# Optimization experiments

Measured on AMD Instinct MI355X. Metric: run time of the kernel, lower is better.

## Reference

```python
import jax, jax.numpy as jnp
import numpy as np

N = 100000      # nodes
E = 3200000     # edges (avg degree 32)
F_IN = 500      # input features
HID = 8         # per-head hidden dim (layer 1)
HEADS = 8       # heads (layer 1)
NC = 41         # num classes (layer 2, 1 head)


def setup_inputs() -> dict:
    key = jax.random.key(0)
    ks = jax.random.split(key, 8)
    x = jax.random.normal(ks[0], (N, F_IN), jnp.float32)
    edge_index = jax.random.randint(ks[1], (2, E), 0, N, dtype=jnp.int64)
    W1 = jax.random.normal(ks[2], (F_IN, HEADS * HID), jnp.float32) / np.sqrt(F_IN)
    a1_src = jax.random.normal(ks[3], (HEADS, HID), jnp.float32) / np.sqrt(HID)
    a1_dst = jax.random.normal(ks[4], (HEADS, HID), jnp.float32) / np.sqrt(HID)
    W2 = jax.random.normal(ks[5], (HEADS * HID, NC), jnp.float32) / np.sqrt(HEADS * HID)
    a2_src = jax.random.normal(ks[6], (1, NC), jnp.float32) / np.sqrt(NC)
    a2_dst = jax.random.normal(ks[7], (1, NC), jnp.float32) / np.sqrt(NC)
    return {"x": x, "edge_index": edge_index, "W1": W1, "a1_src": a1_src,
            "a1_dst": a1_dst, "W2": W2, "a2_src": a2_src, "a2_dst": a2_dst}


def gat_layer(x, edge_index, W, a_src, a_dst, heads, out_dim, concat):
    n = x.shape[0]
    h = (x @ W).reshape(n, heads, out_dim)                    # [N,H,D]
    # per-node attention halves (avoids gathering full features for logits)
    alpha_src = jnp.einsum('nhd,hd->nh', h, a_src)            # [N,H]
    alpha_dst = jnp.einsum('nhd,hd->nh', h, a_dst)            # [N,H]
    src, dst = edge_index[0], edge_index[1]
    e = jax.nn.leaky_relu(alpha_src[src] + alpha_dst[dst], 0.2)  # [E,H]
    # segment softmax over incoming edges of each destination node
    e_max = jax.lax.stop_gradient(jax.ops.segment_max(e, dst, num_segments=n))
    e_exp = jnp.exp(e - e_max[dst])
    denom = jax.ops.segment_sum(e_exp, dst, num_segments=n)
    alpha = e_exp / (denom[dst] + 1e-16)                      # [E,H]
    msg = alpha[:, :, None] * h[src]                          # [E,H,D]
    out = jax.ops.segment_sum(msg, dst, num_segments=n)       # [N,H,D]
    return out.reshape(n, heads * out_dim) if concat else out.mean(axis=1)


def reference(x, edge_index, W1, a1_src, a1_dst, W2, a2_src, a2_dst):
    # dropout layers are identity at inference
    h = gat_layer(x, edge_index, W1, a1_src, a1_dst, HEADS, HID, True)   # [N,64]
    h = jax.nn.elu(h)
    out = gat_layer(h, edge_index, W2, a2_src, a2_dst, 1, NC, False)     # [N,41]
    return jax.nn.log_softmax(out, axis=1)
```

## Files before the change

### kernel.cpp

```cpp
#include <hip/hip_runtime.h>
#include <hip/hip_bf16.h>
#include <math.h>


#define DEV __device__ __forceinline__

constexpr int N_NODES = 100000;
constexpr int N_EDGES = 3200000;
constexpr int F_IN    = 500;
constexpr int HEADS   = 8;
constexpr int HID     = 8;
constexpr int D1      = HEADS * HID;
constexpr int NC      = 41;

constexpr int NB    = 196;
constexpr int BCAP  = 20480;
constexpr int SEPT  = 16;
constexpr int SCHUNK = 256 * SEPT;

constexpr int KPAD  = 512;
constexpr int LROW  = 520;

constexpr int WSTR = 68;

typedef __attribute__((ext_vector_type(8))) short bf16x8;
typedef __attribute__((ext_vector_type(4))) float f32x4;

DEV float bf2f(unsigned short u) {
    return __uint_as_float(((unsigned int)u) << 16);
}
DEV unsigned short f2b(float f) {
    unsigned int u = __float_as_uint(f);
    unsigned int r = (u + 0x7FFFu + ((u >> 16) & 1u)) >> 16;
    return (unsigned short)r;
}
DEV float leaky(float e) { return e > 0.f ? e : 0.2f * e; }
DEV float readlane_f(float v, int l) {
    return __uint_as_float((unsigned int)__builtin_amdgcn_readlane((int)__float_as_uint(v), l));
}

__global__ void k_detect_convert(const void* xraw, const void* eraw,
                                 const void* w1, const void* a1s, const void* a1d,
                                 const void* w2, const void* a2s, const void* a2d,
                                 unsigned short* W1frag, float* A1Sf, float* A1Df,
                                 float* W2f, float* A2Sf, float* A2Df,
                                 int* flags) {
    __shared__ int sf;
    if (threadIdx.x == 0) {
        const unsigned short* xu = (const unsigned short*)xraw;
        int valid = 0;
        for (int i = 0; i < 64; i++) {
            unsigned short v = xu[2 * i];
            int e = (v >> 7) & 0xFF;
            if (e == 0 || (e >= 90 && e <= 150)) valid++;
        }
        int xf32 = (valid < 56) ? 1 : 0;
        const unsigned int* eu = (const unsigned int*)eraw;
        int zeros = 0;
        for (int k = 0; k < 64; k++)
            if (eu[2 * k + 1] == 0u) zeros++;
        int e64 = (zeros == 64) ? 1 : 0;
        flags[0] = xf32;
        flags[1] = e64;
        sf = xf32;
    }
    __syncthreads();
    bool f32 = (sf != 0);
    auto conv = [&](const void* src, float* dst, int n) {
        if (f32) {
            const float* s = (const float*)src;
            for (int i = threadIdx.x; i < n; i += blockDim.x) dst[i] = s[i];
        } else {
            const unsigned short* s = (const unsigned short*)src;
            for (int i = threadIdx.x; i < n; i += blockDim.x) dst[i] = bf2f(s[i]);
        }
    };
    conv(a1s, A1Sf, HEADS * HID);
    conv(a1d, A1Df, HEADS * HID);
    conv(w2, W2f, D1 * NC);
    conv(a2s, A2Sf, NC);
    conv(a2d, A2Df, NC);
    for (int idx = threadIdx.x; idx < 4 * 16 * 64 * 8; idx += blockDim.x) {
        int wid = idx >> 13, kb = (idx >> 9) & 15, ln = (idx >> 3) & 63, j = idx & 7;
        int k = kb * 32 + (ln >> 4) * 8 + j;
        int n = wid * 16 + (ln & 15);
        unsigned short bits = 0;
        if (k < F_IN) {
            if (f32) bits = f2b(((const float*)w1)[k * D1 + n]);
            else     bits = ((const unsigned short*)w1)[k * D1 + n];
        }
        W1frag[idx] = bits;
    }
}

__global__ __launch_bounds__(256) void k_bucket_scatter(const void* eraw, const int* flags,
                                                        int* bucket_cnt, unsigned int* staging) {
    __shared__ int bh[NB];
    const int t = threadIdx.x;
    for (int i = t; i < NB; i += 256) bh[i] = 0;
    __syncthreads();
    const bool e64 = flags[1] != 0;
    const unsigned int* eu = (const unsigned int*)eraw;
    const int e0 = blockIdx.x * SCHUNK;
    int sv[SEPT], dv[SEPT];
#pragma unroll
    for (int k = 0; k < SEPT; k++) {
        int i = e0 + k * 256 + t;
        if (i < N_EDGES) {
            if (e64) { sv[k] = (int)eu[2 * i]; dv[k] = (int)eu[2 * (N_EDGES + i)]; }
            else     { sv[k] = (int)eu[i];     dv[k] = (int)eu[N_EDGES + i]; }
            atomicAdd(&bh[dv[k] >> 9], 1);
        } else dv[k] = -1;
    }
    __syncthreads();
    for (int i = t; i < NB; i += 256) {
        int c = bh[i];
        int base = c ? atomicAdd(&bucket_cnt[i], c) : 0;
        bh[i] = i * BCAP + base;
    }
    __syncthreads();
#pragma unroll
    for (int k = 0; k < SEPT; k++) {
        if (dv[k] >= 0) {
            int b = dv[k] >> 9;
            int slot = atomicAdd(&bh[b], 1);
            staging[slot] = (unsigned)sv[k] | ((unsigned)(dv[k] & 511) << 17);
        }
    }
}

__global__ void k_cscan(const int* bucket_cnt, int* cbase, int* off) {
    __shared__ int s[256];
    int t = threadIdx.x;
    s[t] = (t < NB) ? bucket_cnt[t] : 0;
    __syncthreads();
    for (int o = 1; o < 256; o <<= 1) {
        int v = (t >= o) ? s[t - o] : 0;
        __syncthreads();
        s[t] += v;
        __syncthreads();
    }
    if (t < NB) cbase[t + 1] = s[t];
    if (t == 0) { cbase[0] = 0; off[N_NODES] = N_EDGES; }
}

__global__ __launch_bounds__(512) void k_csr_build(const unsigned int* __restrict__ staging,
                                                   const int* __restrict__ bucket_cnt,
                                                   const int* __restrict__ cbase,
                                                   int* __restrict__ off, int* __restrict__ csr) {
    __shared__ int sdeg[512];
    __shared__ int scur[512];
    const int t = threadIdx.x;
    const int b = blockIdx.x;
    const int n0 = b << 9;
    const int start = b * BCAP;
    const int end = start + bucket_cnt[b];
    const int base = cbase[b];
    sdeg[t] = 0;
    __syncthreads();
    for (int i = start + t; i < end; i += 512)
        atomicAdd(&sdeg[staging[i] >> 17], 1);
    __syncthreads();
    int d = sdeg[t];
    for (int o = 1; o < 512; o <<= 1) {
        int v = (t >= o) ? sdeg[t - o] : 0;
        __syncthreads();
        sdeg[t] += v;
        __syncthreads();
    }
    int excl = sdeg[t] - d;
    if (n0 + t < N_NODES) off[n0 + t] = base + excl;
    scur[t] = base + excl;
    __syncthreads();
    for (int i = start + t; i < end; i += 512) {
        unsigned v = staging[i];
        int slot = atomicAdd(&scur[v >> 17], 1);
        csr[slot] = (int)(v & 0x1FFFFu);
    }
}

__global__ __launch_bounds__(256) void k_gemm1(const void* xraw, const int* flags,
                                               const unsigned short* __restrict__ W1frag,
                                               const float* A1Sf, const float* A1Df,
                                               unsigned short* __restrict__ h1b,
                                               float* __restrict__ as1,
                                               float* __restrict__ ad1) {
    __shared__ unsigned short ldsx[64 * LROW];
    const int t = threadIdx.x;
    const int r0 = blockIdx.x * 64;
    const bool xf32 = flags[0] != 0;
#pragma unroll
    for (int it = 0; it < 32; it++) {
        int s = it * 256 + t;
        int row = s >> 7, c4 = s & 127;
        int row_g = r0 + row;
        ushort4 v = make_ushort4(0, 0, 0, 0);
        if (c4 < 125 && row_g < N_NODES) {
            if (xf32) {
                float4 f = *(const float4*)((const float*)xraw + (size_t)row_g * F_IN + c4 * 4);
                v = make_ushort4(f2b(f.x), f2b(f.y), f2b(f.z), f2b(f.w));
            } else {
                v = *(const ushort4*)((const unsigned short*)xraw + (size_t)row_g * F_IN + c4 * 4);
            }
        }
        *(ushort4*)(ldsx + row * LROW + c4 * 4) = v;
    }
    __syncthreads();

    const int lane = t & 63;
    const int wid = __builtin_amdgcn_readfirstlane(t >> 6);
    const int m = lane & 15, q = lane >> 4;
    f32x4 acc[4] = {{0.f, 0.f, 0.f, 0.f}, {0.f, 0.f, 0.f, 0.f},
                    {0.f, 0.f, 0.f, 0.f}, {0.f, 0.f, 0.f, 0.f}};
    const unsigned short* wf = W1frag + (size_t)wid * 8192;
#pragma unroll 4
    for (int kb = 0; kb < 16; kb++) {
        bf16x8 b = *(const bf16x8*)(wf + (kb * 64 + lane) * 8);
#pragma unroll
        for (int mb = 0; mb < 4; mb++) {
            bf16x8 a = *(const bf16x8*)(ldsx + (mb * 16 + m) * LROW + kb * 32 + q * 8);
            acc[mb] = __builtin_amdgcn_mfma_f32_16x16x32_bf16(a, b, acc[mb], 0, 0, 0);
        }
    }
    const int col = wid * 16 + m;
    const float a_s = A1Sf[col], a_d = A1Df[col];
    const int h = 2 * wid + (m >> 3);
#pragma unroll
    for (int mb = 0; mb < 4; mb++) {
#pragma unroll
        for (int reg = 0; reg < 4; reg++) {
            int gr = r0 + mb * 16 + q * 4 + reg;
            float vacc = acc[mb][reg];
            bool ok = gr < N_NODES;
            if (ok) h1b[(size_t)gr * D1 + col] = f2b(vacc);
            float ts = vacc * a_s, td = vacc * a_d;
            ts += __shfl_xor(ts, 1, 64); td += __shfl_xor(td, 1, 64);
            ts += __shfl_xor(ts, 2, 64); td += __shfl_xor(td, 2, 64);
            ts += __shfl_xor(ts, 4, 64); td += __shfl_xor(td, 4, 64);
            if (ok && (lane & 7) == 0) {
                as1[gr * HEADS + h] = ts;
                ad1[gr * HEADS + h] = td;
            }
        }
    }
}

__global__ __launch_bounds__(256) void k_agg1(const int* __restrict__ csr,
                                              const int* __restrict__ off,
                                              const unsigned short* __restrict__ h1b,
                                              const float* __restrict__ as1,
                                              const float* __restrict__ ad1,
                                              float* __restrict__ h1e) {
    __shared__ float wlds[4][8 * WSTR];
    const int t = threadIdx.x;
    const int lane = t & 63;
    const int n = (blockIdx.x * blockDim.x + t) >> 6;
    if (n >= N_NODES) return;
    const int beg = off[n], end = off[n + 1];
    const int h0 = lane >> 3;
    float* wl = wlds[(t >> 6) & 3];
    const float* wrow = wl + h0 * WSTR;
    const float* adp = ad1 + n * HEADS;
    float acc = 0.f, dsum = 0.f;
    for (int base = beg; base < end; base += 64) {
        const int cnt = min(64, end - base);
        int sl = 0;
        if (lane < cnt) {
            sl = csr[base + lane];
            const float* ap = as1 + sl * HEADS;
            float4 aa = *(const float4*)(ap);
            float4 ab = *(const float4*)(ap + 4);
            wl[0 * WSTR + lane] = __expf(leaky(aa.x + adp[0]));
            wl[1 * WSTR + lane] = __expf(leaky(aa.y + adp[1]));
            wl[2 * WSTR + lane] = __expf(leaky(aa.z + adp[2]));
            wl[3 * WSTR + lane] = __expf(leaky(aa.w + adp[3]));
            wl[4 * WSTR + lane] = __expf(leaky(ab.x + adp[4]));
            wl[5 * WSTR + lane] = __expf(leaky(ab.y + adp[5]));
            wl[6 * WSTR + lane] = __expf(leaky(ab.z + adp[6]));
            wl[7 * WSTR + lane] = __expf(leaky(ab.w + adp[7]));
        }
        asm volatile("s_waitcnt lgkmcnt(0)" ::: "memory");
        int j = 0;
        for (; j + 4 <= cnt; j += 4) {
            int s0 = __builtin_amdgcn_readlane(sl, j);
            int s1 = __builtin_amdgcn_readlane(sl, j + 1);
            int s2 = __builtin_amdgcn_readlane(sl, j + 2);
            int s3 = __builtin_amdgcn_readlane(sl, j + 3);
            float4 wv = *(const float4*)(wrow + j);
            float g0 = bf2f(h1b[(size_t)s0 * D1 + lane]);
            float g1 = bf2f(h1b[(size_t)s1 * D1 + lane]);
            float g2 = bf2f(h1b[(size_t)s2 * D1 + lane]);
            float g3 = bf2f(h1b[(size_t)s3 * D1 + lane]);
            acc = fmaf(wv.x, g0, acc); dsum += wv.x;
            acc = fmaf(wv.y, g1, acc); dsum += wv.y;
            acc = fmaf(wv.z, g2, acc); dsum += wv.z;
            acc = fmaf(wv.w, g3, acc); dsum += wv.w;
        }
        for (; j < cnt; j++) {
            int s = __builtin_amdgcn_readlane(sl, j);
            float w = wrow[j];
            acc = fmaf(w, bf2f(h1b[(size_t)s * D1 + lane]), acc);
            dsum += w;
        }
    }
    float v = acc / (dsum + 1e-16f);
    float o = v > 0.f ? v : (__expf(v) - 1.f);
    h1e[(size_t)n * D1 + lane] = o;
}

__global__ __launch_bounds__(256) void k_gemm2(const float* __restrict__ h1e,
                                               const float* __restrict__ W2f,
                                               const float* __restrict__ A2Sf,
                                               const float* __restrict__ A2Df,
                                               unsigned short* __restrict__ h2b,
                                               float* __restrict__ as2,
                                               float* __restrict__ ad2) {
    const int row = blockIdx.x * blockDim.x + threadIdx.x;
    if (row >= N_NODES) return;
    float acc[NC];
#pragma unroll
    for (int c = 0; c < NC; c++) acc[c] = 0.f;
    const float* xr = h1e + (size_t)row * D1;
    for (int k = 0; k < D1; k += 4) {
        float4 hv = *(const float4*)(xr + k);
#pragma unroll
        for (int c = 0; c < NC; c++) {
            acc[c] = fmaf(hv.x, W2f[(k + 0) * NC + c], acc[c]);
            acc[c] = fmaf(hv.y, W2f[(k + 1) * NC + c], acc[c]);
            acc[c] = fmaf(hv.z, W2f[(k + 2) * NC + c], acc[c]);
            acc[c] = fmaf(hv.w, W2f[(k + 3) * NC + c], acc[c]);
        }
    }
    float ts = 0.f, td = 0.f;
#pragma unroll
    for (int c = 0; c < NC; c++) {
        h2b[(size_t)row * NC + c] = f2b(acc[c]);
        ts = fmaf(acc[c], A2Sf[c], ts);
        td = fmaf(acc[c], A2Df[c], td);
    }
    as2[row] = ts;
    ad2[row] = td;
}

__global__ __launch_bounds__(256) void k_agg2(const int* __restrict__ csr,
                                              const int* __restrict__ off,
                                              const unsigned short* __restrict__ h2b,
                                              const float* __restrict__ as2,
                                              const float* __restrict__ ad2,
                                              const int* flags, void* out) {
    const int lane = threadIdx.x & 63;
    const int n = (blockIdx.x * blockDim.x + threadIdx.x) >> 6;
    if (n >= N_NODES) return;
    const int beg = off[n], end = off[n + 1];
    const float ad = ad2[n];
    const bool act = lane < NC;
    const int cl = act ? lane : 0;
    float acc = 0.f, dsum = 0.f;
    for (int base = beg; base < end; base += 64) {
        const int cnt = min(64, end - base);
        int idx = min(base + lane, N_EDGES - 1);
        int sl = csr[idx];
        float w = __expf(leaky(as2[sl] + ad));
        int j = 0;
        for (; j + 4 <= cnt; j += 4) {
            int s0 = __builtin_amdgcn_readlane(sl, j);
            int s1 = __builtin_amdgcn_readlane(sl, j + 1);
            int s2 = __builtin_amdgcn_readlane(sl, j + 2);
            int s3 = __builtin_amdgcn_readlane(sl, j + 3);
            float w0 = readlane_f(w, j);
            float w1 = readlane_f(w, j + 1);
            float w2 = readlane_f(w, j + 2);
            float w3 = readlane_f(w, j + 3);
            float g0 = bf2f(h2b[(size_t)s0 * NC + cl]);
            float g1 = bf2f(h2b[(size_t)s1 * NC + cl]);
            float g2 = bf2f(h2b[(size_t)s2 * NC + cl]);
            float g3 = bf2f(h2b[(size_t)s3 * NC + cl]);
            acc = fmaf(w0, g0, acc); dsum += w0;
            acc = fmaf(w1, g1, acc); dsum += w1;
            acc = fmaf(w2, g2, acc); dsum += w2;
            acc = fmaf(w3, g3, acc); dsum += w3;
        }
        for (; j < cnt; j++) {
            int s = __builtin_amdgcn_readlane(sl, j);
            float wj = readlane_f(w, j);
            acc = fmaf(wj, bf2f(h2b[(size_t)s * NC + cl]), acc);
            dsum += wj;
        }
    }
    float val = acc / (dsum + 1e-16f);
    float v = act ? val : -INFINITY;
    float m = v;
#pragma unroll
    for (int o = 1; o < 64; o <<= 1) m = fmaxf(m, __shfl_xor(m, o, 64));
    float ex = act ? __expf(val - m) : 0.f;
#pragma unroll
    for (int o = 1; o < 64; o <<= 1) ex += __shfl_xor(ex, o, 64);
    float res = val - m - __logf(ex);
    if (act) {
        if (flags[0])
            ((float*)out)[(size_t)n * NC + lane] = res;
        else
            ((__hip_bfloat16*)out)[(size_t)n * NC + lane] = __float2bfloat16(res);
    }
}

extern "C" void kernel_launch(void* const* d_in, const int* in_sizes, int n_in,
                              void* d_out, int out_size, void* d_ws, size_t ws_size,
                              hipStream_t stream) {
    char* p = (char*)d_ws;
    auto alloc = [&](size_t bytes) -> void* {
        void* r = (void*)p;
        p += (bytes + 255) & ~(size_t)255;
        return r;
    };
    int* flags  = (int*)alloc(16);
    unsigned short* W1frag = (unsigned short*)alloc(4 * 16 * 64 * 8 * 2);
    float* A1Sf = (float*)alloc(HEADS * HID * 4);
    float* A1Df = (float*)alloc(HEADS * HID * 4);
    float* W2f  = (float*)alloc((size_t)D1 * NC * 4);
    float* A2Sf = (float*)alloc(NC * 4);
    float* A2Df = (float*)alloc(NC * 4);
    unsigned short* h1b = (unsigned short*)alloc((size_t)N_NODES * D1 * 2);
    float* as1  = (float*)alloc((size_t)N_NODES * HEADS * 4);
    float* ad1  = (float*)alloc((size_t)N_NODES * HEADS * 4);
    float* h1e  = (float*)alloc((size_t)N_NODES * D1 * 4);
    unsigned short* h2b = (unsigned short*)alloc((size_t)N_NODES * NC * 2);
    float* as2  = (float*)alloc((size_t)N_NODES * 4);
    float* ad2  = (float*)alloc((size_t)N_NODES * 4);
    int* off    = (int*)alloc((size_t)(N_NODES + 1) * 4);
    int* csr    = (int*)alloc((size_t)N_EDGES * 4);
    int* bucket_cnt = (int*)alloc((size_t)NB * 4);
    int* cbase      = (int*)alloc((size_t)(NB + 1) * 4);
    unsigned int* staging = (unsigned int*)h1e;

    hipMemsetAsync(bucket_cnt, 0, (size_t)NB * 4, stream);

    k_detect_convert<<<1, 256, 0, stream>>>(d_in[0], d_in[1], d_in[2], d_in[3],
                                            d_in[4], d_in[5], d_in[6], d_in[7],
                                            W1frag, A1Sf, A1Df, W2f, A2Sf, A2Df, flags);
    k_bucket_scatter<<<(N_EDGES + SCHUNK - 1) / SCHUNK, 256, 0, stream>>>(d_in[1], flags, bucket_cnt, staging);
    k_cscan<<<1, 256, 0, stream>>>(bucket_cnt, cbase, off);
    k_csr_build<<<NB, 512, 0, stream>>>(staging, bucket_cnt, cbase, off, csr);

    k_gemm1<<<1563, 256, 0, stream>>>(d_in[0], flags, W1frag, A1Sf, A1Df, h1b, as1, ad1);
    k_agg1<<<25000, 256, 0, stream>>>(csr, off, h1b, as1, ad1, h1e);
    k_gemm2<<<391, 256, 0, stream>>>(h1e, W2f, A2Sf, A2Df, h2b, as2, ad2);
    k_agg2<<<25000, 256, 0, stream>>>(csr, off, h2b, as2, ad2, flags, d_out);
}
```

Measured before the change: 696.8 us.

## Split detect/convert into parallel kernels and retile gemm1 to 32-row blocks

```diff
diff --git a/kernel.cpp b/kernel.cpp
--- a/kernel.cpp
+++ b/kernel.cpp
@@ -18,7 +18,7 @@
 constexpr int SEPT  = 16;
 constexpr int SCHUNK = 256 * SEPT;
 
-constexpr int KPAD  = 512;
+constexpr int GROWS = 32;
 constexpr int LROW  = 520;
 
 constexpr int WSTR = 68;
@@ -39,48 +39,44 @@
     return __uint_as_float((unsigned int)__builtin_amdgcn_readlane((int)__float_as_uint(v), l));
 }
 
-__global__ void k_detect_convert(const void* xraw, const void* eraw,
-                                 const void* w1, const void* a1s, const void* a1d,
-                                 const void* w2, const void* a2s, const void* a2d,
-                                 unsigned short* W1frag, float* A1Sf, float* A1Df,
-                                 float* W2f, float* A2Sf, float* A2Df,
-                                 int* flags) {
-    __shared__ int sf;
-    if (threadIdx.x == 0) {
-        const unsigned short* xu = (const unsigned short*)xraw;
-        int valid = 0;
-        for (int i = 0; i < 64; i++) {
-            unsigned short v = xu[2 * i];
-            int e = (v >> 7) & 0xFF;
-            if (e == 0 || (e >= 90 && e <= 150)) valid++;
-        }
-        int xf32 = (valid < 56) ? 1 : 0;
-        const unsigned int* eu = (const unsigned int*)eraw;
-        int zeros = 0;
-        for (int k = 0; k < 64; k++)
-            if (eu[2 * k + 1] == 0u) zeros++;
-        int e64 = (zeros == 64) ? 1 : 0;
-        flags[0] = xf32;
-        flags[1] = e64;
-        sf = xf32;
-    }
-    __syncthreads();
-    bool f32 = (sf != 0);
-    auto conv = [&](const void* src, float* dst, int n) {
-        if (f32) {
-            const float* s = (const float*)src;
-            for (int i = threadIdx.x; i < n; i += blockDim.x) dst[i] = s[i];
-        } else {
-            const unsigned short* s = (const unsigned short*)src;
-            for (int i = threadIdx.x; i < n; i += blockDim.x) dst[i] = bf2f(s[i]);
-        }
-    };
-    conv(a1s, A1Sf, HEADS * HID);
-    conv(a1d, A1Df, HEADS * HID);
-    conv(w2, W2f, D1 * NC);
-    conv(a2s, A2Sf, NC);
-    conv(a2d, A2Df, NC);
-    for (int idx = threadIdx.x; idx < 4 * 16 * 64 * 8; idx += blockDim.x) {
+__global__ void k_detect(const void* xraw, const void* eraw, int* flags) {
+    const int lane = threadIdx.x & 63;
+    const unsigned short* xu = (const unsigned short*)xraw;
+    unsigned short v = xu[2 * lane];
+    int e = (v >> 7) & 0xFF;
+    int valid = (e == 0 || (e >= 90 && e <= 150)) ? 1 : 0;
+    unsigned long long vm = __ballot(valid);
+    const unsigned int* eu = (const unsigned int*)eraw;
+    unsigned long long zm = __ballot(eu[2 * lane + 1] == 0u);
+    if (lane == 0) {
+        flags[0] = (__popcll(vm) < 56) ? 1 : 0;
+        flags[1] = (__popcll(zm) == 64) ? 1 : 0;
+    }
+}
+
+__global__ __launch_bounds__(256) void k_convert(const void* w1, const void* a1s, const void* a1d,
+                                                 const void* w2, const void* a2s, const void* a2d,
+                                                 const int* flags,
+                                                 unsigned short* W1frag, float* A1Sf, float* A1Df,
+                                                 float* W2f, float* A2Sf, float* A2Df) {
+    const bool f32 = flags[0] != 0;
+    if (blockIdx.x == 0) {
+        auto conv = [&](const void* src, float* dst, int n) {
+            if (f32) {
+                const float* s = (const float*)src;
+                for (int i = threadIdx.x; i < n; i += blockDim.x) dst[i] = s[i];
+            } else {
+                const unsigned short* s = (const unsigned short*)src;
+                for (int i = threadIdx.x; i < n; i += blockDim.x) dst[i] = bf2f(s[i]);
+            }
+        };
+        conv(a1s, A1Sf, HEADS * HID);
+        conv(a1d, A1Df, HEADS * HID);
+        conv(w2, W2f, D1 * NC);
+        conv(a2s, A2Sf, NC);
+        conv(a2d, A2Df, NC);
+    }
+    for (int idx = blockIdx.x * 256 + threadIdx.x; idx < 4 * 16 * 64 * 8; idx += 64 * 256) {
         int wid = idx >> 13, kb = (idx >> 9) & 15, ln = (idx >> 3) & 63, j = idx & 7;
         int k = kb * 32 + (ln >> 4) * 8 + j;
         int n = wid * 16 + (ln & 15);
@@ -179,23 +175,23 @@
     }
 }
 
-__global__ __launch_bounds__(256) void k_gemm1(const void* xraw, const int* flags,
-                                               const unsigned short* __restrict__ W1frag,
-                                               const float* A1Sf, const float* A1Df,
-                                               unsigned short* __restrict__ h1b,
-                                               float* __restrict__ as1,
-                                               float* __restrict__ ad1) {
-    __shared__ unsigned short ldsx[64 * LROW];
+__global__ __launch_bounds__(512, 8) void k_gemm1(const void* xraw, const int* flags,
+                                                  const unsigned short* __restrict__ W1frag,
+                                                  const float* A1Sf, const float* A1Df,
+                                                  unsigned short* __restrict__ h1b,
+                                                  float* __restrict__ as1,
+                                                  float* __restrict__ ad1) {
+    __shared__ unsigned short ldsx[GROWS * LROW];
     const int t = threadIdx.x;
-    const int r0 = blockIdx.x * 64;
+    const int r0 = blockIdx.x * GROWS;
     const bool xf32 = flags[0] != 0;
-#pragma unroll
-    for (int it = 0; it < 32; it++) {
-        int s = it * 256 + t;
+#pragma unroll 4
+    for (int it = 0; it < 8; it++) {
+        int s = it * 512 + t;
         int row = s >> 7, c4 = s & 127;
         int row_g = r0 + row;
         ushort4 v = make_ushort4(0, 0, 0, 0);
-        if (c4 < 125 && row_g < N_NODES) {
+        if (c4 < 125) {
             if (xf32) {
                 float4 f = *(const float4*)((const float*)xraw + (size_t)row_g * F_IN + c4 * 4);
                 v = make_ushort4(f2b(f.x), f2b(f.y), f2b(f.z), f2b(f.w));
@@ -208,39 +204,34 @@
     __syncthreads();
 
     const int lane = t & 63;
-    const int wid = __builtin_amdgcn_readfirstlane(t >> 6);
+    const int w = t >> 6;
+    const int wid = __builtin_amdgcn_readfirstlane(w & 3);
+    const int mb  = __builtin_amdgcn_readfirstlane(w >> 2);
     const int m = lane & 15, q = lane >> 4;
-    f32x4 acc[4] = {{0.f, 0.f, 0.f, 0.f}, {0.f, 0.f, 0.f, 0.f},
-                    {0.f, 0.f, 0.f, 0.f}, {0.f, 0.f, 0.f, 0.f}};
+    f32x4 acc = {0.f, 0.f, 0.f, 0.f};
     const unsigned short* wf = W1frag + (size_t)wid * 8192;
+    const unsigned short* arow = ldsx + (mb * 16 + m) * LROW + q * 8;
 #pragma unroll 4
     for (int kb = 0; kb < 16; kb++) {
         bf16x8 b = *(const bf16x8*)(wf + (kb * 64 + lane) * 8);
-#pragma unroll
-        for (int mb = 0; mb < 4; mb++) {
-            bf16x8 a = *(const bf16x8*)(ldsx + (mb * 16 + m) * LROW + kb * 32 + q * 8);
-            acc[mb] = __builtin_amdgcn_mfma_f32_16x16x32_bf16(a, b, acc[mb], 0, 0, 0);
-        }
+        bf16x8 a = *(const bf16x8*)(arow + kb * 32);
+        acc = __builtin_amdgcn_mfma_f32_16x16x32_bf16(a, b, acc, 0, 0, 0);
     }
     const int col = wid * 16 + m;
     const float a_s = A1Sf[col], a_d = A1Df[col];
     const int h = 2 * wid + (m >> 3);
 #pragma unroll
-    for (int mb = 0; mb < 4; mb++) {
-#pragma unroll
-        for (int reg = 0; reg < 4; reg++) {
-            int gr = r0 + mb * 16 + q * 4 + reg;
-            float vacc = acc[mb][reg];
-            bool ok = gr < N_NODES;
-            if (ok) h1b[(size_t)gr * D1 + col] = f2b(vacc);
-            float ts = vacc * a_s, td = vacc * a_d;
-            ts += __shfl_xor(ts, 1, 64); td += __shfl_xor(td, 1, 64);
-            ts += __shfl_xor(ts, 2, 64); td += __shfl_xor(td, 2, 64);
-            ts += __shfl_xor(ts, 4, 64); td += __shfl_xor(td, 4, 64);
-            if (ok && (lane & 7) == 0) {
-                as1[gr * HEADS + h] = ts;
-                ad1[gr * HEADS + h] = td;
-            }
+    for (int reg = 0; reg < 4; reg++) {
+        int gr = r0 + mb * 16 + q * 4 + reg;
+        float vacc = acc[reg];
+        h1b[(size_t)gr * D1 + col] = f2b(vacc);
+        float ts = vacc * a_s, td = vacc * a_d;
+        ts += __shfl_xor(ts, 1, 64); td += __shfl_xor(td, 1, 64);
+        ts += __shfl_xor(ts, 2, 64); td += __shfl_xor(td, 2, 64);
+        ts += __shfl_xor(ts, 4, 64); td += __shfl_xor(td, 4, 64);
+        if ((lane & 7) == 0) {
+            as1[gr * HEADS + h] = ts;
+            ad1[gr * HEADS + h] = td;
         }
     }
 }
@@ -435,14 +426,14 @@
 
     hipMemsetAsync(bucket_cnt, 0, (size_t)NB * 4, stream);
 
-    k_detect_convert<<<1, 256, 0, stream>>>(d_in[0], d_in[1], d_in[2], d_in[3],
-                                            d_in[4], d_in[5], d_in[6], d_in[7],
-                                            W1frag, A1Sf, A1Df, W2f, A2Sf, A2Df, flags);
+    k_detect<<<1, 64, 0, stream>>>(d_in[0], d_in[1], flags);
+    k_convert<<<64, 256, 0, stream>>>(d_in[2], d_in[3], d_in[4], d_in[5], d_in[6], d_in[7],
+                                      flags, W1frag, A1Sf, A1Df, W2f, A2Sf, A2Df);
     k_bucket_scatter<<<(N_EDGES + SCHUNK - 1) / SCHUNK, 256, 0, stream>>>(d_in[1], flags, bucket_cnt, staging);
     k_cscan<<<1, 256, 0, stream>>>(bucket_cnt, cbase, off);
     k_csr_build<<<NB, 512, 0, stream>>>(staging, bucket_cnt, cbase, off, csr);
 
-    k_gemm1<<<1563, 256, 0, stream>>>(d_in[0], flags, W1frag, A1Sf, A1Df, h1b, as1, ad1);
+    k_gemm1<<<(N_NODES + GROWS - 1) / GROWS, 512, 0, stream>>>(d_in[0], flags, W1frag, A1Sf, A1Df, h1b, as1, ad1);
     k_agg1<<<25000, 256, 0, stream>>>(csr, off, h1b, as1, ad1, h1e);
     k_gemm2<<<391, 256, 0, stream>>>(h1e, W2f, A2Sf, A2Df, h2b, as2, ad2);
     k_agg2<<<25000, 256, 0, stream>>>(csr, off, h2b, as2, ad2, flags, d_out);
```

Result: faster. 614.5 us (-11.8%).
